# Performance work log

Measured on AMD Instinct MI355X. Metric: run time of the kernel, lower is better.

## Reference

```python
import jax, jax.numpy as jnp
import numpy as np

B, I, H = 8192, 1024, 1024

def _xavier(key, out_f, in_f):
    limit = (6.0 / (in_f + out_f)) ** 0.5
    return jax.random.uniform(key, (out_f, in_f), jnp.float32, -limit, limit)

def setup_inputs() -> dict:
    key = jax.random.key(0)
    ks = jax.random.split(key, 11)
    inp = {
        'x': jax.random.normal(ks[0], (B, I), jnp.float32),
        'h': jax.random.normal(ks[1], (B, H), jnp.float32),
        'c': jax.random.normal(ks[2], (B, H), jnp.float32),
    }
    names = ['Wxi', 'Whi', 'Wxf', 'Whf', 'Wxo', 'Who', 'Wxg', 'Whg']
    for n, k in zip(names, ks[3:]):
        in_f = I if n[1] == 'x' else H
        inp[n + '_w'] = _xavier(k, H, in_f)
        inp[n + '_b'] = jnp.zeros((H,), jnp.float32)
    return inp

def reference(x, h, c,
              Wxi_w, Wxi_b, Whi_w, Whi_b,
              Wxf_w, Wxf_b, Whf_w, Whf_b,
              Wxo_w, Wxo_b, Who_w, Who_b,
              Wxg_w, Wxg_b, Whg_w, Whg_b):
    Wx = jnp.concatenate([Wxi_w, Wxf_w, Wxo_w, Wxg_w], axis=0)  # [4H, I]
    Wh = jnp.concatenate([Whi_w, Whf_w, Who_w, Whg_w], axis=0)  # [4H, H]
    bx = jnp.concatenate([Wxi_b, Wxf_b, Wxo_b, Wxg_b], axis=0)  # [4H]
    bh = jnp.concatenate([Whi_b, Whf_b, Who_b, Whg_b], axis=0)  # [4H]
    z = x @ Wx.T + bx + h @ Wh.T + bh  # [B, 4H]
    zi, zf, zo, zg = jnp.split(z, 4, axis=-1)
    it = jax.nn.sigmoid(zi)
    ft = jax.nn.sigmoid(zf)
    ot = jax.nn.sigmoid(zo)
    gt = jnp.tanh(zg)
    c_next = ft * c + it * gt
    h_next = ot * jnp.tanh(c_next)
    return (h_next, c_next)
```

## Files before the change

### kernel.cpp

```cpp
#include <hip/hip_runtime.h>
#include <hip/hip_bf16.h>
#include <cstdint>


typedef __bf16 bf16;
typedef __attribute__((ext_vector_type(8))) bf16 bf16x8;
typedef __attribute__((ext_vector_type(4))) float f32x4;

#define CN_OFF 8388608

__device__ __forceinline__ void gload16(const bf16* g, bf16* l) {
  __builtin_amdgcn_global_load_lds(
      (const __attribute__((address_space(1))) void*)g,
      (__attribute__((address_space(3))) void*)l, 16, 0, 0);
}

__device__ __forceinline__ bf16x8 cvt8(f32x4 v0, f32x4 v1) {
  bf16x8 o;
  o[0]=(bf16)v0[0]; o[1]=(bf16)v0[1]; o[2]=(bf16)v0[2]; o[3]=(bf16)v0[3];
  o[4]=(bf16)v1[0]; o[5]=(bf16)v1[1]; o[6]=(bf16)v1[2]; o[7]=(bf16)v1[3];
  return o;
}

__global__ __launch_bounds__(256) void pack_all(
    const float* __restrict__ x, const float* __restrict__ h,
    const float* __restrict__ wxi, const float* __restrict__ whi,
    const float* __restrict__ wxf, const float* __restrict__ whf,
    const float* __restrict__ wxo, const float* __restrict__ who,
    const float* __restrict__ wxg, const float* __restrict__ whg,
    const float* __restrict__ bxi, const float* __restrict__ bhi,
    const float* __restrict__ bxf, const float* __restrict__ bhf,
    const float* __restrict__ bxo, const float* __restrict__ bho,
    const float* __restrict__ bxg, const float* __restrict__ bhg,
    bf16* __restrict__ A2, bf16* __restrict__ B2, float* __restrict__ Bcomb) {
  __shared__ __align__(16) bf16 lds[8192];
  const int t = threadIdx.x;
  const int bid = blockIdx.x;

  if (bid < 2048) {
    const int mb = bid >> 5;
    const int wm = (bid >> 4) & 1;
    const int q  = bid & 15;
    const int rowbase = mb * 128 + wm * 64;
    const float* srcM; int k0;
    if (q < 8) { srcM = x; k0 = q * 128; } else { srcM = h; k0 = q * 128 - 1024; }
#pragma unroll
    for (int r = 0; r < 4; ++r) {
      const int rl = r * 16 + (t >> 4);
      const int cc = (t & 15) * 8;
      const float* s = srcM + (size_t)(rowbase + rl) * 1024 + k0 + cc;
      f32x4 v0 = *(const f32x4*)s;
      f32x4 v1 = *(const f32x4*)(s + 4);
      const int chunkS = (t & 15) ^ (rl & 7);
      *(bf16x8*)((char*)lds + rl * 256 + chunkS * 16) = cvt8(v0, v1);
    }
    __syncthreads();
#pragma unroll
    for (int r = 0; r < 4; ++r) {
      const int idx = r * 256 + t;
      const int fj  = idx >> 6;
      const int ktL = fj >> 2, mi = fj & 3;
      const int l   = idx & 63;
      const int srow = mi * 16 + (l & 15);
      const int chunkS = (ktL * 4 + (l >> 4)) ^ (srow & 7);
      bf16x8 o = *(const bf16x8*)((const char*)lds + srow * 256 + chunkS * 16);
      size_t el = ((size_t)mb * 64 + q * 4 + ktL) * 4096 + (size_t)wm * 2048 + mi * 512 + l * 8;
      *(bf16x8*)(A2 + el) = o;
    }
  } else {
    const int bid2 = bid - 2048;
    const int nb   = bid2 >> 6;
    const int gate = (bid2 >> 4) & 3;
    const int q    = bid2 & 15;
    const float* wxm = (gate == 0) ? wxi : (gate == 1) ? wxf : (gate == 2) ? wxo : wxg;
    const float* whm = (gate == 0) ? whi : (gate == 1) ? whf : (gate == 2) ? who : whg;
    const float* srcM; int k0;
    if (q < 8) { srcM = wxm; k0 = q * 128; } else { srcM = whm; k0 = q * 128 - 1024; }
    const int jbase = nb * 32;
#pragma unroll
    for (int r = 0; r < 2; ++r) {
      const int rl = r * 16 + (t >> 4);
      const int cc = (t & 15) * 8;
      const float* s = srcM + (size_t)(jbase + rl) * 1024 + k0 + cc;
      f32x4 v0 = *(const f32x4*)s;
      f32x4 v1 = *(const f32x4*)(s + 4);
      const int chunkS = (t & 15) ^ (rl & 7);
      *(bf16x8*)((char*)lds + rl * 256 + chunkS * 16) = cvt8(v0, v1);
    }
    __syncthreads();
#pragma unroll
    for (int r = 0; r < 2; ++r) {
      const int idx = r * 256 + t;
      const int fj  = idx >> 6;
      const int ktL = fj >> 1, wn = fj & 1;
      const int l   = idx & 63;
      const int srow = wn * 16 + (l & 15);
      const int chunkS = (ktL * 4 + (l >> 4)) ^ (srow & 7);
      bf16x8 o = *(const bf16x8*)((const char*)lds + srow * 256 + chunkS * 16);
      size_t el = ((size_t)nb * 64 + q * 4 + ktL) * 4096 + (size_t)wn * 2048 + gate * 512 + l * 8;
      *(bf16x8*)(B2 + el) = o;
    }
    if (q == 0 && t < 32) {
      const float* bxv = (gate == 0) ? bxi : (gate == 1) ? bxf : (gate == 2) ? bxo : bxg;
      const float* bhv = (gate == 0) ? bhi : (gate == 1) ? bhf : (gate == 2) ? bho : bhg;
      const int wn = t >> 4, jl = t & 15;
      const int j = nb * 32 + wn * 16 + jl;
      Bcomb[(nb * 2 + wn) * 64 + gate * 16 + jl] = bxv[j] + bhv[j];
    }
  }
}

__device__ __forceinline__ float sigf(float v) { return 1.f / (1.f + __expf(-v)); }
__device__ __forceinline__ float tanhfast(float v) {
  v = fminf(15.f, fmaxf(-15.f, v));
  float e = __expf(2.f * v);
  return (e - 1.f) / (e + 1.f);
}

__global__ __launch_bounds__(512, 4) void gemm_lstm(const bf16* __restrict__ A2,
                                                    const bf16* __restrict__ B2,
                                                    const float* __restrict__ Bcomb,
                                                    const float* __restrict__ c,
                                                    float* __restrict__ out) {
  __shared__ __align__(16) bf16 lds[36864];
  const int t    = threadIdx.x;
  const int wave = t >> 6;
  const int lane = t & 63;

  const int bid = blockIdx.x;
  const int xcd = bid & 7;
  const int idx = bid >> 3;
  const int nb  = xcd * 4 + (idx & 3);
  const int bm  = idx >> 2;

  const int wr  = wave >> 1;
  const int wn  = wave & 1;
  const int mbU = wr >> 1, wm = wr & 1;
  const int lrow = lane & 15, lkg = lane >> 4;

  const int tEl = t * 8;
  const int wEl = (t & ~63) * 8;

  const bf16* aSrc0 = A2 + (size_t)(2 * bm)     * 64 * 4096;
  const bf16* aSrc1 = A2 + (size_t)(2 * bm + 1) * 64 * 4096;
  const bf16* bSrc  = B2 + (size_t)nb           * 64 * 4096;

  auto stage = [&](int tile, int buf) {
    const size_t kOff = (size_t)tile * 4096;
    bf16* d = lds + buf * 12288;
    gload16(aSrc0 + kOff + tEl, d +        wEl);
    gload16(aSrc1 + kOff + tEl, d + 4096 + wEl);
    gload16(bSrc  + kOff + tEl, d + 8192 + wEl);
  };

  f32x4 acc[4][4] = {};

  stage(0, 0);
  stage(1, 1);

  const int aOff = mbU * 4096 + wm * 2048 + lane * 8;
  const int bOff = 8192 + wn * 2048 + lane * 8;

  auto body = [&](int kt, int p, int pn, bool doStage, bool last) {
    if (last) asm volatile("s_waitcnt vmcnt(0)" ::: "memory");
    else      asm volatile("s_waitcnt vmcnt(3)" ::: "memory");
    __builtin_amdgcn_s_barrier();
    asm volatile("" ::: "memory");
    if (doStage) stage(kt + 2, pn);
    const bf16* bufA = lds + p * 12288 + aOff;
    const bf16* bufB = lds + p * 12288 + bOff;
    bf16x8 af[4], bfr[4];
#pragma unroll
    for (int i = 0; i < 4; ++i)
      af[i] = *(const bf16x8*)(bufA + i * 512);
#pragma unroll
    for (int g = 0; g < 4; ++g)
      bfr[g] = *(const bf16x8*)(bufB + g * 512);
    __builtin_amdgcn_s_setprio(1);
#pragma unroll
    for (int mi = 0; mi < 4; ++mi)
#pragma unroll
      for (int g = 0; g < 4; ++g)
        acc[mi][g] = __builtin_amdgcn_mfma_f32_16x16x32_bf16(af[mi], bfr[g], acc[mi][g], 0, 0, 0);
    __builtin_amdgcn_s_setprio(0);
  };

#pragma unroll 1
  for (int base = 0; base < 63; base += 3) {
    body(base,     0, 2, base     < 62, false);
    body(base + 1, 1, 0, base + 1 < 62, false);
    body(base + 2, 2, 1, base + 2 < 62, false);
  }
  body(63, 0, 0, false, true);

  const int jg = (nb * 2 + wn) * 16 + lrow;
  const int bbase = (nb * 2 + wn) * 64 + lrow;
  const float bi  = Bcomb[bbase +  0];
  const float bf_ = Bcomb[bbase + 16];
  const float bo  = Bcomb[bbase + 32];
  const float bg  = Bcomb[bbase + 48];

#pragma unroll
  for (int mi = 0; mi < 4; ++mi) {
    const int row0 = bm * 256 + mbU * 128 + wm * 64 + mi * 16 + lkg * 4;
    float cv[4];
#pragma unroll
    for (int r = 0; r < 4; ++r)
      cv[r] = c[(size_t)(row0 + r) * 1024 + jg];
#pragma unroll
    for (int r = 0; r < 4; ++r) {
      float zi = acc[mi][0][r] + bi;
      float zf = acc[mi][1][r] + bf_;
      float zo = acc[mi][2][r] + bo;
      float zg = acc[mi][3][r] + bg;
      float it = sigf(zi), ft = sigf(zf), ot = sigf(zo), gt = tanhfast(zg);
      float cn = ft * cv[r] + it * gt;
      size_t off = (size_t)(row0 + r) * 1024 + jg;
      out[off] = ot * tanhfast(cn);
      out[CN_OFF + off] = cn;
    }
  }
}

extern "C" void kernel_launch(void* const* d_in, const int* in_sizes, int n_in,
                              void* d_out, int out_size, void* d_ws, size_t ws_size,
                              hipStream_t stream) {
  const float* x   = (const float*)d_in[0];
  const float* h   = (const float*)d_in[1];
  const float* c   = (const float*)d_in[2];
  const float* Wxi = (const float*)d_in[3];  const float* bxi = (const float*)d_in[4];
  const float* Whi = (const float*)d_in[5];  const float* bhi = (const float*)d_in[6];
  const float* Wxf = (const float*)d_in[7];  const float* bxf = (const float*)d_in[8];
  const float* Whf = (const float*)d_in[9];  const float* bhf = (const float*)d_in[10];
  const float* Wxo = (const float*)d_in[11]; const float* bxo = (const float*)d_in[12];
  const float* Who = (const float*)d_in[13]; const float* bho = (const float*)d_in[14];
  const float* Wxg = (const float*)d_in[15]; const float* bxg = (const float*)d_in[16];
  const float* Whg = (const float*)d_in[17]; const float* bhg = (const float*)d_in[18];
  float* out = (float*)d_out;

  bf16*  Abuf  = (bf16*)d_ws;
  bf16*  Wbuf  = Abuf + (size_t)8192 * 2048;
  float* Bcomb = (float*)(Wbuf + (size_t)4096 * 2048);

  pack_all<<<4096, 256, 0, stream>>>(x, h,
                                     Wxi, Whi, Wxf, Whf, Wxo, Who, Wxg, Whg,
                                     bxi, bhi, bxf, bhf, bxo, bho, bxg, bhg,
                                     Abuf, Wbuf, Bcomb);
  gemm_lstm<<<1024, 512, 0, stream>>>(Abuf, Wbuf, Bcomb, c, out);
}
```

Baseline: 314.7 us.

## Load B fragments directly from global into registers, prefetching one tile ahead

The weight (B) tile no longer goes through LDS. Each wave reads its B fragments straight from global memory into registers, double-buffered one k-tile ahead, while A keeps its three-stage LDS pipeline. This cuts LDS size and traffic and removes the LDS reads for B. The cost is more VGPR pressure, and each wave pair now loads its own B fragments from global/L2 where the block used to share them, with a different vmcnt wait accounting.

Result: slower. 527.1 us (+67.5%).

```diff
diff --git a/kernel.cpp b/kernel.cpp
--- a/kernel.cpp
+++ b/kernel.cpp
@@ -122,7 +122,7 @@
                                                     const float* __restrict__ Bcomb,
                                                     const float* __restrict__ c,
                                                     float* __restrict__ out) {
-  __shared__ __align__(16) bf16 lds[36864];
+  __shared__ __align__(16) bf16 lds[24576];
   const int t    = threadIdx.x;
   const int wave = t >> 6;
   const int lane = t & 63;
@@ -143,55 +143,61 @@
 
   const bf16* aSrc0 = A2 + (size_t)(2 * bm)     * 64 * 4096;
   const bf16* aSrc1 = A2 + (size_t)(2 * bm + 1) * 64 * 4096;
-  const bf16* bSrc  = B2 + (size_t)nb           * 64 * 4096;
-
-  auto stage = [&](int tile, int buf) {
+  const bf16* bW    = B2 + (size_t)nb * 64 * 4096 + wn * 2048 + lane * 8;
+
+  auto stageA = [&](int tile, int buf) {
     const size_t kOff = (size_t)tile * 4096;
-    bf16* d = lds + buf * 12288;
+    bf16* d = lds + buf * 8192;
     gload16(aSrc0 + kOff + tEl, d +        wEl);
     gload16(aSrc1 + kOff + tEl, d + 4096 + wEl);
-    gload16(bSrc  + kOff + tEl, d + 8192 + wEl);
   };
 
   f32x4 acc[4][4] = {};
-
-  stage(0, 0);
-  stage(1, 1);
+  bf16x8 bCur[4], bNxt[4];
+
+  stageA(0, 0);
+  stageA(1, 1);
+#pragma unroll
+  for (int g = 0; g < 4; ++g)
+    bCur[g] = *(const bf16x8*)(bW + g * 512);
 
   const int aOff = mbU * 4096 + wm * 2048 + lane * 8;
-  const int bOff = 8192 + wn * 2048 + lane * 8;
-
-  auto body = [&](int kt, int p, int pn, bool doStage, bool last) {
+
+  auto body = [&](int kt, int p, int pn, bool doStage, bool doB, bool last) {
     if (last) asm volatile("s_waitcnt vmcnt(0)" ::: "memory");
-    else      asm volatile("s_waitcnt vmcnt(3)" ::: "memory");
+    else      asm volatile("s_waitcnt vmcnt(6)" ::: "memory");
     __builtin_amdgcn_s_barrier();
     asm volatile("" ::: "memory");
-    if (doStage) stage(kt + 2, pn);
-    const bf16* bufA = lds + p * 12288 + aOff;
-    const bf16* bufB = lds + p * 12288 + bOff;
-    bf16x8 af[4], bfr[4];
+    if (doStage) stageA(kt + 2, pn);
+    const bf16* bufA = lds + p * 8192 + aOff;
+    bf16x8 af[4];
 #pragma unroll
     for (int i = 0; i < 4; ++i)
       af[i] = *(const bf16x8*)(bufA + i * 512);
-#pragma unroll
-    for (int g = 0; g < 4; ++g)
-      bfr[g] = *(const bf16x8*)(bufB + g * 512);
+    if (doB) {
+      const bf16* bp = bW + (size_t)(kt + 1) * 4096;
+#pragma unroll
+      for (int g = 0; g < 4; ++g)
+        bNxt[g] = *(const bf16x8*)(bp + g * 512);
+    }
     __builtin_amdgcn_s_setprio(1);
 #pragma unroll
     for (int mi = 0; mi < 4; ++mi)
 #pragma unroll
       for (int g = 0; g < 4; ++g)
-        acc[mi][g] = __builtin_amdgcn_mfma_f32_16x16x32_bf16(af[mi], bfr[g], acc[mi][g], 0, 0, 0);
+        acc[mi][g] = __builtin_amdgcn_mfma_f32_16x16x32_bf16(af[mi], bCur[g], acc[mi][g], 0, 0, 0);
     __builtin_amdgcn_s_setprio(0);
+#pragma unroll
+    for (int g = 0; g < 4; ++g) bCur[g] = bNxt[g];
   };
 
 #pragma unroll 1
   for (int base = 0; base < 63; base += 3) {
-    body(base,     0, 2, base     < 62, false);
-    body(base + 1, 1, 0, base + 1 < 62, false);
-    body(base + 2, 2, 1, base + 2 < 62, false);
+    body(base,     0, 2, base     < 62, true, false);
+    body(base + 1, 1, 0, base + 1 < 62, true, false);
+    body(base + 2, 2, 1, base + 2 < 62, base + 2 < 63, false);
   }
-  body(63, 0, 0, false, true);
+  body(63, 0, 0, false, false, true);
 
   const int jg = (nb * 2 + wn) * 16 + lrow;
   const int bbase = (nb * 2 + wn) * 64 + lrow;
```

## Fuse pack and GEMM kernels into one persistent launch with a grid barrier

Applied to the files above, without the earlier changes.

Merges the bf16 pack kernel and the LSTM GEMM kernel into one 512-block kernel. Each block first packs its share of A and B tiles, then all blocks meet at a global atomic-counter barrier, and each block then computes two N-tiles in sequence. This removes a kernel launch and the gap between kernels. In exchange it adds a memset launch and a spin-wait barrier that deadlocks unless all 512 blocks are co-resident, and it runs the GEMM tiles serially per block over half as many blocks.

After: 563.0 us. 1.79x slower.

```diff
diff --git a/kernel.cpp b/kernel.cpp
--- a/kernel.cpp
+++ b/kernel.cpp
@@ -22,7 +22,14 @@
   return o;
 }
 
-__global__ __launch_bounds__(256) void pack_all(
+__device__ __forceinline__ float sigf(float v) { return 1.f / (1.f + __expf(-v)); }
+__device__ __forceinline__ float tanhfast(float v) {
+  v = fminf(15.f, fmaxf(-15.f, v));
+  float e = __expf(2.f * v);
+  return (e - 1.f) / (e + 1.f);
+}
+
+__global__ __launch_bounds__(512, 4) void lstm_fused(
     const float* __restrict__ x, const float* __restrict__ h,
     const float* __restrict__ wxi, const float* __restrict__ whi,
     const float* __restrict__ wxf, const float* __restrict__ whf,
@@ -32,192 +39,204 @@
     const float* __restrict__ bxf, const float* __restrict__ bhf,
     const float* __restrict__ bxo, const float* __restrict__ bho,
     const float* __restrict__ bxg, const float* __restrict__ bhg,
-    bf16* __restrict__ A2, bf16* __restrict__ B2, float* __restrict__ Bcomb) {
-  __shared__ __align__(16) bf16 lds[8192];
-  const int t = threadIdx.x;
+    const float* __restrict__ c, float* __restrict__ out,
+    bf16* __restrict__ A2, bf16* __restrict__ B2, float* __restrict__ Bcomb,
+    unsigned int* __restrict__ cnt) {
+  __shared__ __align__(16) bf16 lds[36864];
+  const int t   = threadIdx.x;
   const int bid = blockIdx.x;
 
-  if (bid < 2048) {
-    const int mb = bid >> 5;
-    const int wm = (bid >> 4) & 1;
-    const int q  = bid & 15;
-    const int rowbase = mb * 128 + wm * 64;
-    const float* srcM; int k0;
-    if (q < 8) { srcM = x; k0 = q * 128; } else { srcM = h; k0 = q * 128 - 1024; }
-#pragma unroll
-    for (int r = 0; r < 4; ++r) {
-      const int rl = r * 16 + (t >> 4);
-      const int cc = (t & 15) * 8;
-      const float* s = srcM + (size_t)(rowbase + rl) * 1024 + k0 + cc;
-      f32x4 v0 = *(const f32x4*)s;
-      f32x4 v1 = *(const f32x4*)(s + 4);
-      const int chunkS = (t & 15) ^ (rl & 7);
-      *(bf16x8*)((char*)lds + rl * 256 + chunkS * 16) = cvt8(v0, v1);
-    }
-    __syncthreads();
-#pragma unroll
-    for (int r = 0; r < 4; ++r) {
-      const int idx = r * 256 + t;
-      const int fj  = idx >> 6;
-      const int ktL = fj >> 2, mi = fj & 3;
-      const int l   = idx & 63;
-      const int srow = mi * 16 + (l & 15);
-      const int chunkS = (ktL * 4 + (l >> 4)) ^ (srow & 7);
-      bf16x8 o = *(const bf16x8*)((const char*)lds + srow * 256 + chunkS * 16);
-      size_t el = ((size_t)mb * 64 + q * 4 + ktL) * 4096 + (size_t)wm * 2048 + mi * 512 + l * 8;
-      *(bf16x8*)(A2 + el) = o;
-    }
-  } else {
-    const int bid2 = bid - 2048;
-    const int nb   = bid2 >> 6;
-    const int gate = (bid2 >> 4) & 3;
-    const int q    = bid2 & 15;
-    const float* wxm = (gate == 0) ? wxi : (gate == 1) ? wxf : (gate == 2) ? wxo : wxg;
-    const float* whm = (gate == 0) ? whi : (gate == 1) ? whf : (gate == 2) ? who : whg;
-    const float* srcM; int k0;
-    if (q < 8) { srcM = wxm; k0 = q * 128; } else { srcM = whm; k0 = q * 128 - 1024; }
-    const int jbase = nb * 32;
-#pragma unroll
-    for (int r = 0; r < 2; ++r) {
-      const int rl = r * 16 + (t >> 4);
-      const int cc = (t & 15) * 8;
-      const float* s = srcM + (size_t)(jbase + rl) * 1024 + k0 + cc;
-      f32x4 v0 = *(const f32x4*)s;
-      f32x4 v1 = *(const f32x4*)(s + 4);
-      const int chunkS = (t & 15) ^ (rl & 7);
-      *(bf16x8*)((char*)lds + rl * 256 + chunkS * 16) = cvt8(v0, v1);
-    }
-    __syncthreads();
-#pragma unroll
-    for (int r = 0; r < 2; ++r) {
-      const int idx = r * 256 + t;
-      const int fj  = idx >> 6;
-      const int ktL = fj >> 1, wn = fj & 1;
-      const int l   = idx & 63;
-      const int srow = wn * 16 + (l & 15);
-      const int chunkS = (ktL * 4 + (l >> 4)) ^ (srow & 7);
-      bf16x8 o = *(const bf16x8*)((const char*)lds + srow * 256 + chunkS * 16);
-      size_t el = ((size_t)nb * 64 + q * 4 + ktL) * 4096 + (size_t)wn * 2048 + gate * 512 + l * 8;
-      *(bf16x8*)(B2 + el) = o;
-    }
-    if (q == 0 && t < 32) {
-      const float* bxv = (gate == 0) ? bxi : (gate == 1) ? bxf : (gate == 2) ? bxo : bxg;
-      const float* bhv = (gate == 0) ? bhi : (gate == 1) ? bhf : (gate == 2) ? bho : bhg;
-      const int wn = t >> 4, jl = t & 15;
-      const int j = nb * 32 + wn * 16 + jl;
-      Bcomb[(nb * 2 + wn) * 64 + gate * 16 + jl] = bxv[j] + bhv[j];
+  {
+    const int g  = t >> 8;
+    const int ts = t & 255;
+    bf16* ldsg = lds + g * 8192;
+
+#pragma unroll 1
+    for (int it = 0; it < 2; ++it) {
+      const int uA = bid * 4 + g * 2 + it;
+      const int mb = uA >> 5;
+      const int wm = (uA >> 4) & 1;
+      const int q  = uA & 15;
+      const int rowbase = mb * 128 + wm * 64;
+      const float* srcM; int k0;
+      if (q < 8) { srcM = x; k0 = q * 128; } else { srcM = h; k0 = q * 128 - 1024; }
+#pragma unroll
+      for (int r = 0; r < 4; ++r) {
+        const int rl = r * 16 + (ts >> 4);
+        const int cc = (ts & 15) * 8;
+        const float* s = srcM + (size_t)(rowbase + rl) * 1024 + k0 + cc;
+        f32x4 v0 = *(const f32x4*)s;
+        f32x4 v1 = *(const f32x4*)(s + 4);
+        const int chunkS = (ts & 15) ^ (rl & 7);
+        *(bf16x8*)((char*)ldsg + rl * 256 + chunkS * 16) = cvt8(v0, v1);
+      }
+      __syncthreads();
+#pragma unroll
+      for (int r = 0; r < 4; ++r) {
+        const int idx = r * 256 + ts;
+        const int fj  = idx >> 6;
+        const int ktL = fj >> 2, mi = fj & 3;
+        const int l   = idx & 63;
+        const int srow = mi * 16 + (l & 15);
+        const int chunkS = (ktL * 4 + (l >> 4)) ^ (srow & 7);
+        bf16x8 o = *(const bf16x8*)((const char*)ldsg + srow * 256 + chunkS * 16);
+        size_t el = ((size_t)mb * 64 + q * 4 + ktL) * 4096 + (size_t)wm * 2048 + mi * 512 + l * 8;
+        *(bf16x8*)(A2 + el) = o;
+      }
+      __syncthreads();
+    }
+
+#pragma unroll 1
+    for (int it = 0; it < 2; ++it) {
+      const int uB = bid * 4 + g * 2 + it;
+      const int nb   = uB >> 6;
+      const int gate = (uB >> 4) & 3;
+      const int q    = uB & 15;
+      const float* wxm = (gate == 0) ? wxi : (gate == 1) ? wxf : (gate == 2) ? wxo : wxg;
+      const float* whm = (gate == 0) ? whi : (gate == 1) ? whf : (gate == 2) ? who : whg;
+      const float* srcM; int k0;
+      if (q < 8) { srcM = wxm; k0 = q * 128; } else { srcM = whm; k0 = q * 128 - 1024; }
+      const int jbase = nb * 32;
+#pragma unroll
+      for (int r = 0; r < 2; ++r) {
+        const int rl = r * 16 + (ts >> 4);
+        const int cc = (ts & 15) * 8;
+        const float* s = srcM + (size_t)(jbase + rl) * 1024 + k0 + cc;
+        f32x4 v0 = *(const f32x4*)s;
+        f32x4 v1 = *(const f32x4*)(s + 4);
+        const int chunkS = (ts & 15) ^ (rl & 7);
+        *(bf16x8*)((char*)ldsg + rl * 256 + chunkS * 16) = cvt8(v0, v1);
+      }
+      __syncthreads();
+#pragma unroll
+      for (int r = 0; r < 2; ++r) {
+        const int idx = r * 256 + ts;
+        const int fj  = idx >> 6;
+        const int ktL = fj >> 1, wn = fj & 1;
+        const int l   = idx & 63;
+        const int srow = wn * 16 + (l & 15);
+        const int chunkS = (ktL * 4 + (l >> 4)) ^ (srow & 7);
+        bf16x8 o = *(const bf16x8*)((const char*)ldsg + srow * 256 + chunkS * 16);
+        size_t el = ((size_t)nb * 64 + q * 4 + ktL) * 4096 + (size_t)wn * 2048 + gate * 512 + l * 8;
+        *(bf16x8*)(B2 + el) = o;
+      }
+      if (q == 0 && ts < 32) {
+        const float* bxv = (gate == 0) ? bxi : (gate == 1) ? bxf : (gate == 2) ? bxo : bxg;
+        const float* bhv = (gate == 0) ? bhi : (gate == 1) ? bhf : (gate == 2) ? bho : bhg;
+        const int wn = ts >> 4, jl = ts & 15;
+        const int j = nb * 32 + wn * 16 + jl;
+        Bcomb[(nb * 2 + wn) * 64 + gate * 16 + jl] = bxv[j] + bhv[j];
+      }
+      __syncthreads();
     }
   }
-}
-
-__device__ __forceinline__ float sigf(float v) { return 1.f / (1.f + __expf(-v)); }
-__device__ __forceinline__ float tanhfast(float v) {
-  v = fminf(15.f, fmaxf(-15.f, v));
-  float e = __expf(2.f * v);
-  return (e - 1.f) / (e + 1.f);
-}
-
-__global__ __launch_bounds__(512, 4) void gemm_lstm(const bf16* __restrict__ A2,
-                                                    const bf16* __restrict__ B2,
-                                                    const float* __restrict__ Bcomb,
-                                                    const float* __restrict__ c,
-                                                    float* __restrict__ out) {
-  __shared__ __align__(16) bf16 lds[36864];
-  const int t    = threadIdx.x;
+
+  __syncthreads();
+  __threadfence();
+  if (t == 0) {
+    atomicAdd(cnt, 1u);
+    while (__hip_atomic_load(cnt, __ATOMIC_ACQUIRE, __HIP_MEMORY_SCOPE_AGENT) < 512u)
+      __builtin_amdgcn_s_sleep(2);
+  }
+  __syncthreads();
+
   const int wave = t >> 6;
   const int lane = t & 63;
-
-  const int bid = blockIdx.x;
   const int xcd = bid & 7;
   const int idx = bid >> 3;
-  const int nb  = xcd * 4 + (idx & 3);
-  const int bm  = idx >> 2;
+  const int nbP = xcd * 2 + (idx & 1);
+  const int bm  = idx >> 1;
 
   const int wr  = wave >> 1;
   const int wn  = wave & 1;
-  const int mbU = wr >> 1, wm = wr & 1;
+  const int mbU = wr >> 1, wm2 = wr & 1;
   const int lrow = lane & 15, lkg = lane >> 4;
 
   const int tEl = t * 8;
   const int wEl = (t & ~63) * 8;
 
-  const bf16* aSrc0 = A2 + (size_t)(2 * bm)     * 64 * 4096;
-  const bf16* aSrc1 = A2 + (size_t)(2 * bm + 1) * 64 * 4096;
-  const bf16* bSrc  = B2 + (size_t)nb           * 64 * 4096;
-
-  auto stage = [&](int tile, int buf) {
-    const size_t kOff = (size_t)tile * 4096;
-    bf16* d = lds + buf * 12288;
-    gload16(aSrc0 + kOff + tEl, d +        wEl);
-    gload16(aSrc1 + kOff + tEl, d + 4096 + wEl);
-    gload16(bSrc  + kOff + tEl, d + 8192 + wEl);
-  };
-
-  f32x4 acc[4][4] = {};
-
-  stage(0, 0);
-  stage(1, 1);
-
-  const int aOff = mbU * 4096 + wm * 2048 + lane * 8;
+  const bf16* aSrc0 = A2 + (size_t)(2 * bm)     * 262144;
+  const bf16* aSrc1 = A2 + (size_t)(2 * bm + 1) * 262144;
+  const int aOff = mbU * 4096 + wm2 * 2048 + lane * 8;
   const int bOff = 8192 + wn * 2048 + lane * 8;
 
-  auto body = [&](int kt, int p, int pn, bool doStage, bool last) {
-    if (last) asm volatile("s_waitcnt vmcnt(0)" ::: "memory");
-    else      asm volatile("s_waitcnt vmcnt(3)" ::: "memory");
-    __builtin_amdgcn_s_barrier();
-    asm volatile("" ::: "memory");
-    if (doStage) stage(kt + 2, pn);
-    const bf16* bufA = lds + p * 12288 + aOff;
-    const bf16* bufB = lds + p * 12288 + bOff;
-    bf16x8 af[4], bfr[4];
-#pragma unroll
-    for (int i = 0; i < 4; ++i)
-      af[i] = *(const bf16x8*)(bufA + i * 512);
-#pragma unroll
-    for (int g = 0; g < 4; ++g)
-      bfr[g] = *(const bf16x8*)(bufB + g * 512);
-    __builtin_amdgcn_s_setprio(1);
-#pragma unroll
-    for (int mi = 0; mi < 4; ++mi)
+#pragma unroll 1
+  for (int tl = 0; tl < 2; ++tl) {
+    const int nb = nbP * 2 + tl;
+    const bf16* bSrc = B2 + (size_t)nb * 262144;
+
+    auto stage = [&](int tile, int buf) {
+      const size_t kOff = (size_t)tile * 4096;
+      bf16* d = lds + buf * 12288;
+      gload16(aSrc0 + kOff + tEl, d +        wEl);
+      gload16(aSrc1 + kOff + tEl, d + 4096 + wEl);
+      gload16(bSrc  + kOff + tEl, d + 8192 + wEl);
+    };
+
+    f32x4 acc[4][4] = {};
+
+    __syncthreads();
+    stage(0, 0);
+    stage(1, 1);
+
+    auto body = [&](int kt, int p, int pn, bool doStage, bool last) {
+      if (last) asm volatile("s_waitcnt vmcnt(0)" ::: "memory");
+      else      asm volatile("s_waitcnt vmcnt(3)" ::: "memory");
+      __builtin_amdgcn_s_barrier();
+      asm volatile("" ::: "memory");
+      if (doStage) stage(kt + 2, pn);
+      const bf16* bufA = lds + p * 12288 + aOff;
+      const bf16* bufB = lds + p * 12288 + bOff;
+      bf16x8 af[4], bfr[4];
+#pragma unroll
+      for (int i = 0; i < 4; ++i)
+        af[i] = *(const bf16x8*)(bufA + i * 512);
 #pragma unroll
       for (int g = 0; g < 4; ++g)
-        acc[mi][g] = __builtin_amdgcn_mfma_f32_16x16x32_bf16(af[mi], bfr[g], acc[mi][g], 0, 0, 0);
-    __builtin_amdgcn_s_setprio(0);
-  };
-
-#pragma unroll 1
-  for (int base = 0; base < 63; base += 3) {
-    body(base,     0, 2, base     < 62, false);
-    body(base + 1, 1, 0, base + 1 < 62, false);
-    body(base + 2, 2, 1, base + 2 < 62, false);
-  }
-  body(63, 0, 0, false, true);
-
-  const int jg = (nb * 2 + wn) * 16 + lrow;
-  const int bbase = (nb * 2 + wn) * 64 + lrow;
-  const float bi  = Bcomb[bbase +  0];
-  const float bf_ = Bcomb[bbase + 16];
-  const float bo  = Bcomb[bbase + 32];
-  const float bg  = Bcomb[bbase + 48];
-
-#pragma unroll
-  for (int mi = 0; mi < 4; ++mi) {
-    const int row0 = bm * 256 + mbU * 128 + wm * 64 + mi * 16 + lkg * 4;
-    float cv[4];
-#pragma unroll
-    for (int r = 0; r < 4; ++r)
-      cv[r] = c[(size_t)(row0 + r) * 1024 + jg];
-#pragma unroll
-    for (int r = 0; r < 4; ++r) {
-      float zi = acc[mi][0][r] + bi;
-      float zf = acc[mi][1][r] + bf_;
-      float zo = acc[mi][2][r] + bo;
-      float zg = acc[mi][3][r] + bg;
-      float it = sigf(zi), ft = sigf(zf), ot = sigf(zo), gt = tanhfast(zg);
-      float cn = ft * cv[r] + it * gt;
-      size_t off = (size_t)(row0 + r) * 1024 + jg;
-      out[off] = ot * tanhfast(cn);
-      out[CN_OFF + off] = cn;
+        bfr[g] = *(const bf16x8*)(bufB + g * 512);
+      __builtin_amdgcn_s_setprio(1);
+#pragma unroll
+      for (int mi = 0; mi < 4; ++mi)
+#pragma unroll
+        for (int g = 0; g < 4; ++g)
+          acc[mi][g] = __builtin_amdgcn_mfma_f32_16x16x32_bf16(af[mi], bfr[g], acc[mi][g], 0, 0, 0);
+      __builtin_amdgcn_s_setprio(0);
+    };
+
+#pragma unroll 1
+    for (int base = 0; base < 63; base += 3) {
+      body(base,     0, 2, base     < 62, false);
+      body(base + 1, 1, 0, base + 1 < 62, false);
+      body(base + 2, 2, 1, base + 2 < 62, false);
+    }
+    body(63, 0, 0, false, true);
+
+    const int jg = (nb * 2 + wn) * 16 + lrow;
+    const int bbase = (nb * 2 + wn) * 64 + lrow;
+    const float bi  = Bcomb[bbase +  0];
+    const float bf_ = Bcomb[bbase + 16];
+    const float bo  = Bcomb[bbase + 32];
+    const float bg  = Bcomb[bbase + 48];
+
+#pragma unroll
+    for (int mi = 0; mi < 4; ++mi) {
+      const int row0 = bm * 256 + mbU * 128 + wm2 * 64 + mi * 16 + lkg * 4;
+      float cv[4];
+#pragma unroll
+      for (int r = 0; r < 4; ++r)
+        cv[r] = c[(size_t)(row0 + r) * 1024 + jg];
+#pragma unroll
+      for (int r = 0; r < 4; ++r) {
+        float zi = acc[mi][0][r] + bi;
+        float zf = acc[mi][1][r] + bf_;
+        float zo = acc[mi][2][r] + bo;
+        float zg = acc[mi][3][r] + bg;
+        float it = sigf(zi), ft = sigf(zf), ot = sigf(zo), gt = tanhfast(zg);
+        float cn = ft * cv[r] + it * gt;
+        size_t off = (size_t)(row0 + r) * 1024 + jg;
+        out[off] = ot * tanhfast(cn);
+        out[CN_OFF + off] = cn;
+      }
     }
   }
 }
@@ -241,10 +260,11 @@
   bf16*  Abuf  = (bf16*)d_ws;
   bf16*  Wbuf  = Abuf + (size_t)8192 * 2048;
   float* Bcomb = (float*)(Wbuf + (size_t)4096 * 2048);
-
-  pack_all<<<4096, 256, 0, stream>>>(x, h,
-                                     Wxi, Whi, Wxf, Whf, Wxo, Who, Wxg, Whg,
-                                     bxi, bhi, bxf, bhf, bxo, bho, bxg, bhg,
-                                     Abuf, Wbuf, Bcomb);
-  gemm_lstm<<<1024, 512, 0, stream>>>(Abuf, Wbuf, Bcomb, c, out);
-}
+  unsigned int* cnt = (unsigned int*)(Bcomb + 4096);
+
+  hipMemsetAsync(cnt, 0, sizeof(unsigned int), stream);
+  lstm_fused<<<512, 512, 0, stream>>>(x, h,
+                                      Wxi, Whi, Wxf, Whf, Wxo, Who, Wxg, Whg,
+                                      bxi, bhi, bxf, bhf, bxo, bho, bxg, bhg,
+                                      c, out, Abuf, Wbuf, Bcomb, cnt);
+}
```
